# Kernel tuning notes

Measured on AMD Instinct MI355X. Metric: run time of the kernel, lower is better.

Reference implementation:

```python
import jax, jax.numpy as jnp
import numpy as np

EMBED_DIM = 1024
NUM_HEADS = 16
HEAD_DIM = EMBED_DIM // NUM_HEADS
B, S = 2, 2048


def setup_inputs() -> dict:
    key = jax.random.key(0)
    ks = jax.random.split(key, 9)
    s = 1.0 / np.sqrt(EMBED_DIM)
    return {
        "x": jax.random.normal(ks[0], (B, S, EMBED_DIM), dtype=jnp.float32),
        "Wq": jax.random.normal(ks[1], (EMBED_DIM, EMBED_DIM), dtype=jnp.float32) * s,
        "bq": jnp.zeros((EMBED_DIM,), dtype=jnp.float32),
        "Wk": jax.random.normal(ks[2], (EMBED_DIM, EMBED_DIM), dtype=jnp.float32) * s,
        "bk": jnp.zeros((EMBED_DIM,), dtype=jnp.float32),
        "Wv": jax.random.normal(ks[3], (EMBED_DIM, EMBED_DIM), dtype=jnp.float32) * s,
        "bv": jnp.zeros((EMBED_DIM,), dtype=jnp.float32),
        "Wo": jax.random.normal(ks[4], (EMBED_DIM, EMBED_DIM), dtype=jnp.float32) * s,
        "bo": jnp.zeros((EMBED_DIM,), dtype=jnp.float32),
    }


def reference(x, Wq, bq, Wk, bk, Wv, bv, Wo, bo):
    b, s, _ = x.shape
    # Projections; reshape to [B, H, S, Dh]
    def proj(W, bias):
        return (x @ W + bias).reshape(b, s, NUM_HEADS, HEAD_DIM).transpose(0, 2, 1, 3)
    q = proj(Wq, bq)
    k = proj(Wk, bk)
    v = proj(Wv, bv)
    scale = 1.0 / np.sqrt(HEAD_DIM).astype(np.float32)
    scores = jnp.einsum('bhqd,bhkd->bhqk', q, k) * scale  # [B,H,S,S]
    attn = jax.nn.softmax(scores, axis=-1)
    out = jnp.einsum('bhqk,bhkd->bhqd', attn, v)  # [B,H,S,Dh]
    out = out.transpose(0, 2, 1, 3).reshape(b, s, EMBED_DIM)
    return out @ Wo + bo
```

## Files before the change

kernel.cpp:

```cpp
#include <hip/hip_runtime.h>
#include <hip/hip_bf16.h>

typedef unsigned short ushort_t;
typedef __attribute__((ext_vector_type(8))) short short8;
typedef __attribute__((ext_vector_type(4))) float f32x4;
typedef __attribute__((ext_vector_type(16))) float f32x16;
typedef __attribute__((ext_vector_type(2))) unsigned int uint2v;

#define EMBED 1024
#define NHEAD 16
#define HDIM 64
#define BB 2
#define SSEQ 2048
#define MROWS (BB*SSEQ)
#define QKV_N (3*EMBED)
#define PER_BUF (MROWS*EMBED)

__device__ __forceinline__ ushort_t f2bf(float f) {
    union { float f; unsigned int u; } x; x.f = f;
    unsigned int r = x.u + 0x7fffu + ((x.u >> 16) & 1u);
    return (ushort_t)(r >> 16);
}
__device__ __forceinline__ unsigned cvt_pk_bf16(float lo, float hi) {
    unsigned r;
    asm("v_cvt_pk_bf16_f32 %0, %1, %2" : "=v"(r) : "v"(lo), "v"(hi));
    return r;
}

__device__ __forceinline__ void gload16(const void* g, void* l) {
    __builtin_amdgcn_global_load_lds(
        (const __attribute__((address_space(1))) unsigned int*)g,
        (__attribute__((address_space(3))) unsigned int*)l, 16, 0, 0);
}

__global__ void cast_bf16_kernel(const float* __restrict__ in, ushort_t* __restrict__ out, int n) {
    int i = (blockIdx.x * blockDim.x + threadIdx.x) * 4;
    if (i + 3 < n) {
        float4 v = *(const float4*)(in + i);
        out[i+0] = f2bf(v.x); out[i+1] = f2bf(v.y);
        out[i+2] = f2bf(v.z); out[i+3] = f2bf(v.w);
    }
}

__global__ void transpose_cast4_kernel(
    const float* __restrict__ W0, const float* __restrict__ W1,
    const float* __restrict__ W2, const float* __restrict__ W3,
    ushort_t* __restrict__ T0, ushort_t* __restrict__ T1,
    ushort_t* __restrict__ T2, ushort_t* __restrict__ T3)
{
    __shared__ float tile[32][33];
    int z = blockIdx.z;
    const float* W = (z == 0) ? W0 : (z == 1) ? W1 : (z == 2) ? W2 : W3;
    ushort_t* Wt   = (z == 0) ? T0 : (z == 1) ? T1 : (z == 2) ? T2 : T3;
    int tx = threadIdx.x, ty = threadIdx.y;
    int n0 = blockIdx.x * 32, k0 = blockIdx.y * 32;
    #pragma unroll
    for (int i = 0; i < 4; i++)
        tile[ty*4+i][tx] = W[(size_t)(k0 + ty*4 + i) * EMBED + n0 + tx];
    __syncthreads();
    #pragma unroll
    for (int i = 0; i < 4; i++)
        Wt[(size_t)(n0 + ty*4 + i) * EMBED + k0 + tx] = f2bf(tile[tx][ty*4+i]);
}

__global__ void transpose_v_kernel(const ushort_t* __restrict__ v, ushort_t* __restrict__ vt) {
    __shared__ ushort_t tile[64][66];
    int bh = blockIdx.y, s0 = blockIdx.x * 64;
    int t = threadIdx.x;
    int r = t >> 3, c8 = (t & 7) * 8;
    #pragma unroll
    for (int p = 0; p < 2; p++) {
        short8 vv = *(const short8*)&v[((size_t)bh*SSEQ + s0 + p*32 + r)*HDIM + c8];
        #pragma unroll
        for (int j = 0; j < 8; j++) tile[p*32 + r][c8 + j] = (ushort_t)vv[j];
    }
    __syncthreads();
    #pragma unroll
    for (int p = 0; p < 2; p++) {
        int d = p*32 + r;
        short8 ov;
        #pragma unroll
        for (int j = 0; j < 8; j++) ov[j] = (short)tile[c8 + j][d];
        *(short8*)&vt[((size_t)bh*HDIM + d)*SSEQ + s0 + c8] = ov;
    }
}

template<int OUT_MODE>
__global__ __launch_bounds__(256) void gemm_bt_kernel(
    const ushort_t* __restrict__ A,
    const ushort_t* __restrict__ Bt,
    const float* __restrict__ b0, const float* __restrict__ b1, const float* __restrict__ b2,
    void* __restrict__ Cout,
    int M, int N, int K)
{
    __shared__ __attribute__((aligned(16))) ushort_t Asm[128*64];
    __shared__ __attribute__((aligned(16))) ushort_t Bsm[128*64];
    int t = threadIdx.x;
    int w = t >> 6, l = t & 63;
    int wr = w >> 1, wc = w & 1;
    int lrow = l & 15, lhi = l >> 4;

    int gx = gridDim.x;
    int flat = blockIdx.y * gx + blockIdx.x;
    int q8 = (gx * gridDim.y) >> 3;
    int nf = (flat & 7) * q8 + (flat >> 3);
    int m0 = (nf / gx) * 128, n0 = (nf % gx) * 128;

    int srow8 = l >> 3;
    int colel = 8 * ((l & 7) ^ srow8);

    f32x4 acc[4][4];
    #pragma unroll
    for (int mi = 0; mi < 4; mi++)
        #pragma unroll
        for (int ni = 0; ni < 4; ni++)
            #pragma unroll
            for (int c = 0; c < 4; c++) acc[mi][ni][c] = 0.f;

    for (int k0 = 0; k0 < K; k0 += 64) {
        __syncthreads();
        #pragma unroll
        for (int p = 0; p < 4; p++) {
            int row = w*32 + p*8 + srow8;
            gload16(&A [(size_t)(m0 + row)*K + k0 + colel], &Asm[(w*32 + p*8)*64]);
            gload16(&Bt[(size_t)(n0 + row)*K + k0 + colel], &Bsm[(w*32 + p*8)*64]);
        }
        __syncthreads();
        #pragma unroll
        for (int kk = 0; kk < 2; kk++) {
            short8 af[4], bfr[4];
            #pragma unroll
            for (int mi = 0; mi < 4; mi++) {
                int r = wr*64 + mi*16 + lrow;
                af[mi] = *(short8*)&Asm[r*64 + ((kk*32 + lhi*8) ^ ((r & 7) << 3))];
            }
            #pragma unroll
            for (int ni = 0; ni < 4; ni++) {
                int r = wc*64 + ni*16 + lrow;
                bfr[ni] = *(short8*)&Bsm[r*64 + ((kk*32 + lhi*8) ^ ((r & 7) << 3))];
            }
            __builtin_amdgcn_s_setprio(1);
            #pragma unroll
            for (int mi = 0; mi < 4; mi++)
                #pragma unroll
                for (int ni = 0; ni < 4; ni++)
                    acc[mi][ni] = __builtin_amdgcn_mfma_f32_16x16x32_bf16(af[mi], bfr[ni], acc[mi][ni], 0, 0, 0);
            __builtin_amdgcn_s_setprio(0);
        }
    }

    #pragma unroll
    for (int mi = 0; mi < 4; mi++)
        #pragma unroll
        for (int ni = 0; ni < 4; ni++) {
            int col = n0 + wc*64 + ni*16 + lrow;
            #pragma unroll
            for (int c = 0; c < 4; c++) {
                int row = m0 + wr*64 + mi*16 + lhi*4 + c;
                if (OUT_MODE == 0) {
                    float v = acc[mi][ni][c] + b0[col];
                    ((float*)Cout)[(size_t)row * N + col] = v;
                } else {
                    int which = col >> 10, hc = col & 1023;
                    const float* bp = (which == 0) ? b0 : (which == 1) ? b1 : b2;
                    float v = acc[mi][ni][c] + bp[hc];
                    if (which == 0) v *= 0.18033688011112042f;
                    int h = hc >> 6, d = hc & 63;
                    int b = row >> 11, s = row & 2047;
                    ((ushort_t*)Cout)[(size_t)which*PER_BUF + ((size_t)((b*NHEAD + h)*SSEQ) + s)*HDIM + d] = f2bf(v);
                }
            }
        }
}

#define MFMA32(a,b,c) __builtin_amdgcn_mfma_f32_32x32x16_bf16(a, b, c, 0, 0, 0)

__global__ __launch_bounds__(256, 2) void flash_attn2_kernel(
    const ushort_t* __restrict__ q,
    const ushort_t* __restrict__ k,
    const ushort_t* __restrict__ vt,
    ushort_t* __restrict__ o)
{
    __shared__ __attribute__((aligned(16))) ushort_t Ks[2][2][64*64];
    __shared__ __attribute__((aligned(16))) ushort_t Vs[2][2][64*64];

    int t = threadIdx.x, w = t >> 6, l = t & 63;
    int l31 = l & 31, hi = l >> 5;

    int flat = blockIdx.x;
    int wg = (flat & 7) * 64 + (flat >> 3);
    int bh = wg >> 4;
    int q0 = (wg & 15) * 128;

    const ushort_t* qp = q  + (size_t)bh * SSEQ * HDIM;
    const ushort_t* kp = k  + (size_t)bh * SSEQ * HDIM;
    const ushort_t* vp = vt + (size_t)bh * HDIM * SSEQ;

    int lr = l >> 3, lc = l & 7;
    int colel = 8 * (lc ^ lr);

    short8 qf[4];
    int qrow = q0 + w*32 + l31;
    #pragma unroll
    for (int st = 0; st < 4; st++)
        qf[st] = *(const short8*)&qp[(size_t)qrow*HDIM + st*16 + hi*8];

    f32x16 o0 = {}, o1 = {};
    float m_run = -1e30f, l_run = 0.f;

    #define STAGE(buf, kv0) { \
        _Pragma("unroll") \
        for (int sub = 0; sub < 2; sub++) { \
            _Pragma("unroll") \
            for (int c = 0; c < 2; c++) { \
                int row = w*16 + c*8 + lr; \
                gload16(&kp[(size_t)(kv0 + sub*64 + row)*HDIM + colel], &Ks[buf][sub][(w*16 + c*8)*64]); \
                gload16(&vp[(size_t)row*SSEQ + (kv0) + sub*64 + colel], &Vs[buf][sub][(w*16 + c*8)*64]); \
            } } }

    STAGE(0, 0)
    asm volatile("s_waitcnt vmcnt(0)");
    __syncthreads();
    int cur = 0;

    for (int kv0 = 0; kv0 < SSEQ; kv0 += 128) {
        if (kv0 + 128 < SSEQ) { STAGE(cur ^ 1, kv0 + 128) }

        f32x16 s0 = {}, s1 = {}, s2 = {}, s3 = {};
        __builtin_amdgcn_s_setprio(1);
        #pragma unroll
        for (int st = 0; st < 4; st++) {
            int colb = st*16 + hi*8;
            int sw0 = colb ^ ((l31 & 7) << 3);
            short8 kf0 = *(const short8*)&Ks[cur][0][l31*64        + sw0];
            short8 kf1 = *(const short8*)&Ks[cur][0][(32 + l31)*64 + sw0];
            short8 kf2 = *(const short8*)&Ks[cur][1][l31*64        + sw0];
            short8 kf3 = *(const short8*)&Ks[cur][1][(32 + l31)*64 + sw0];
            s0 = MFMA32(kf0, qf[st], s0);
            s1 = MFMA32(kf1, qf[st], s1);
            s2 = MFMA32(kf2, qf[st], s2);
            s3 = MFMA32(kf3, qf[st], s3);
        }
        __builtin_amdgcn_s_setprio(0);

        float ma = fmaxf(s0[0], s0[1]);
        float mb = fmaxf(s0[2], s0[3]);
        float mc = fmaxf(s0[4], s0[5]);
        float md = fmaxf(s0[6], s0[7]);
        ma = fmaxf(fmaxf(ma, s0[8]),  s0[9]);
        mb = fmaxf(fmaxf(mb, s0[10]), s0[11]);
        mc = fmaxf(fmaxf(mc, s0[12]), s0[13]);
        md = fmaxf(fmaxf(md, s0[14]), s0[15]);
        ma = fmaxf(fmaxf(ma, s1[0]),  s1[1]);
        mb = fmaxf(fmaxf(mb, s1[2]),  s1[3]);
        mc = fmaxf(fmaxf(mc, s1[4]),  s1[5]);
        md = fmaxf(fmaxf(md, s1[6]),  s1[7]);
        ma = fmaxf(fmaxf(ma, s1[8]),  s1[9]);
        mb = fmaxf(fmaxf(mb, s1[10]), s1[11]);
        mc = fmaxf(fmaxf(mc, s1[12]), s1[13]);
        md = fmaxf(fmaxf(md, s1[14]), s1[15]);
        ma = fmaxf(fmaxf(ma, s2[0]),  s2[1]);
        mb = fmaxf(fmaxf(mb, s2[2]),  s2[3]);
        mc = fmaxf(fmaxf(mc, s2[4]),  s2[5]);
        md = fmaxf(fmaxf(md, s2[6]),  s2[7]);
        ma = fmaxf(fmaxf(ma, s2[8]),  s2[9]);
        mb = fmaxf(fmaxf(mb, s2[10]), s2[11]);
        mc = fmaxf(fmaxf(mc, s2[12]), s2[13]);
        md = fmaxf(fmaxf(md, s2[14]), s2[15]);
        ma = fmaxf(fmaxf(ma, s3[0]),  s3[1]);
        mb = fmaxf(fmaxf(mb, s3[2]),  s3[3]);
        mc = fmaxf(fmaxf(mc, s3[4]),  s3[5]);
        md = fmaxf(fmaxf(md, s3[6]),  s3[7]);
        ma = fmaxf(fmaxf(ma, s3[8]),  s3[9]);
        mb = fmaxf(fmaxf(mb, s3[10]), s3[11]);
        mc = fmaxf(fmaxf(mc, s3[12]), s3[13]);
        md = fmaxf(fmaxf(md, s3[14]), s3[15]);
        float mx = fmaxf(fmaxf(ma, mb), fmaxf(mc, md));
        mx = fmaxf(mx, __shfl_xor(mx, 32));

        if (__any(mx > m_run + 8.f)) {
            float mnew = fmaxf(m_run, mx);
            float alpha = __builtin_amdgcn_exp2f(m_run - mnew);
            #pragma unroll
            for (int r = 0; r < 16; r++) { o0[r] *= alpha; o1[r] *= alpha; }
            l_run *= alpha;
            m_run = mnew;
        }
        float r0 = 0.f, r1 = 0.f, r2 = 0.f, r3 = 0.f;
        #pragma unroll
        for (int r = 0; r < 16; r += 4) {
            s0[r]   = __builtin_amdgcn_exp2f(s0[r]   - m_run); r0 += s0[r];
            s0[r+1] = __builtin_amdgcn_exp2f(s0[r+1] - m_run); r1 += s0[r+1];
            s0[r+2] = __builtin_amdgcn_exp2f(s0[r+2] - m_run); r2 += s0[r+2];
            s0[r+3] = __builtin_amdgcn_exp2f(s0[r+3] - m_run); r3 += s0[r+3];
        }
        #pragma unroll
        for (int r = 0; r < 16; r += 4) {
            s1[r]   = __builtin_amdgcn_exp2f(s1[r]   - m_run); r0 += s1[r];
            s1[r+1] = __builtin_amdgcn_exp2f(s1[r+1] - m_run); r1 += s1[r+1];
            s1[r+2] = __builtin_amdgcn_exp2f(s1[r+2] - m_run); r2 += s1[r+2];
            s1[r+3] = __builtin_amdgcn_exp2f(s1[r+3] - m_run); r3 += s1[r+3];
        }
        #pragma unroll
        for (int r = 0; r < 16; r += 4) {
            s2[r]   = __builtin_amdgcn_exp2f(s2[r]   - m_run); r0 += s2[r];
            s2[r+1] = __builtin_amdgcn_exp2f(s2[r+1] - m_run); r1 += s2[r+1];
            s2[r+2] = __builtin_amdgcn_exp2f(s2[r+2] - m_run); r2 += s2[r+2];
            s2[r+3] = __builtin_amdgcn_exp2f(s2[r+3] - m_run); r3 += s2[r+3];
        }
        #pragma unroll
        for (int r = 0; r < 16; r += 4) {
            s3[r]   = __builtin_amdgcn_exp2f(s3[r]   - m_run); r0 += s3[r];
            s3[r+1] = __builtin_amdgcn_exp2f(s3[r+1] - m_run); r1 += s3[r+1];
            s3[r+2] = __builtin_amdgcn_exp2f(s3[r+2] - m_run); r2 += s3[r+2];
            s3[r+3] = __builtin_amdgcn_exp2f(s3[r+3] - m_run); r3 += s3[r+3];
        }
        float rs = (r0 + r1) + (r2 + r3);
        rs += __shfl_xor(rs, 32);
        l_run += rs;

        short8 pfr[8];
        #define PACK8(SV, KS0) { \
            unsigned a0 = cvt_pk_bf16(SV[0], SV[1]); \
            unsigned a1 = cvt_pk_bf16(SV[2], SV[3]); \
            unsigned b0 = cvt_pk_bf16(SV[4], SV[5]); \
            unsigned b1 = cvt_pk_bf16(SV[6], SV[7]); \
            uint2v rr0 = __builtin_amdgcn_permlane32_swap(a0, b0, false, false); \
            uint2v rr1 = __builtin_amdgcn_permlane32_swap(a1, b1, false, false); \
            union { unsigned u[4]; short8 v; } pfa; \
            pfa.u[0] = rr0.x; pfa.u[1] = rr1.x; pfa.u[2] = rr0.y; pfa.u[3] = rr1.y; \
            pfr[KS0] = pfa.v; \
            unsigned c0 = cvt_pk_bf16(SV[8], SV[9]); \
            unsigned c1 = cvt_pk_bf16(SV[10], SV[11]); \
            unsigned d0 = cvt_pk_bf16(SV[12], SV[13]); \
            unsigned d1 = cvt_pk_bf16(SV[14], SV[15]); \
            uint2v rr2 = __builtin_amdgcn_permlane32_swap(c0, d0, false, false); \
            uint2v rr3 = __builtin_amdgcn_permlane32_swap(c1, d1, false, false); \
            union { unsigned u[4]; short8 v; } pfb; \
            pfb.u[0] = rr2.x; pfb.u[1] = rr3.x; pfb.u[2] = rr2.y; pfb.u[3] = rr3.y; \
            pfr[(KS0)+1] = pfb.v; \
        }
        PACK8(s0, 0)
        PACK8(s1, 2)
        PACK8(s2, 4)
        PACK8(s3, 6)
        #undef PACK8

        __builtin_amdgcn_s_setprio(1);
        #pragma unroll
        for (int ks = 0; ks < 8; ks++) {
            int sub = ks >> 2;
            int colb = (ks & 3)*16 + hi*8;
            int sw = colb ^ ((l31 & 7) << 3);
            short8 vf0 = *(const short8*)&Vs[cur][sub][l31*64        + sw];
            short8 vf1 = *(const short8*)&Vs[cur][sub][(32 + l31)*64 + sw];
            o0 = MFMA32(vf0, pfr[ks], o0);
            o1 = MFMA32(vf1, pfr[ks], o1);
        }
        __builtin_amdgcn_s_setprio(0);

        asm volatile("s_waitcnt vmcnt(0)");
        __syncthreads();
        cur ^= 1;
    }

    float rl = 1.f / l_run;
    ushort_t* Ot = ((ushort_t*)Ks) + w*(32*64);
    #pragma unroll
    for (int dt = 0; dt < 2; dt++)
        #pragma unroll
        for (int rq = 0; rq < 4; rq++) {
            float v0 = (dt ? o1[rq*4+0] : o0[rq*4+0]) * rl;
            float v1 = (dt ? o1[rq*4+1] : o0[rq*4+1]) * rl;
            float v2 = (dt ? o1[rq*4+2] : o0[rq*4+2]) * rl;
            float v3 = (dt ? o1[rq*4+3] : o0[rq*4+3]) * rl;
            int d0 = dt*32 + rq*8 + hi*4;
            uint2v pw = { cvt_pk_bf16(v0, v1), cvt_pk_bf16(v2, v3) };
            *(uint2v*)&Ot[l31*64 + (d0 ^ ((l31 & 7) << 3))] = pw;
        }

    int b = bh >> 4, h = bh & 15;
    int q2 = l >> 1, dh = (l & 1) * 32;
    size_t obase = ((size_t)(b*SSEQ) + q0 + w*32 + q2)*EMBED + h*HDIM;
    #pragma unroll
    for (int j = 0; j < 4; j++) {
        int d = dh + j*8;
        short8 ov = *(short8*)&Ot[q2*64 + (d ^ ((q2 & 7) << 3))];
        *(short8*)&o[obase + d] = ov;
    }
}

extern "C" void kernel_launch(void* const* d_in, const int* in_sizes, int n_in,
                              void* d_out, int out_size, void* d_ws, size_t ws_size,
                              hipStream_t stream) {
    const float* x  = (const float*)d_in[0];
    const float* Wq = (const float*)d_in[1];
    const float* bq = (const float*)d_in[2];
    const float* Wk = (const float*)d_in[3];
    const float* bk = (const float*)d_in[4];
    const float* Wv = (const float*)d_in[5];
    const float* bv = (const float*)d_in[6];
    const float* Wo = (const float*)d_in[7];
    const float* bo = (const float*)d_in[8];

    char* ws = (char*)d_ws;
    ushort_t* xb  = (ushort_t*)(ws);
    ushort_t* WqT = (ushort_t*)(ws + (8u  << 20));
    ushort_t* WkT = (ushort_t*)(ws + (10u << 20));
    ushort_t* WvT = (ushort_t*)(ws + (12u << 20));
    ushort_t* WoT = (ushort_t*)(ws + (14u << 20));
    ushort_t* qb  = (ushort_t*)(ws + (16u << 20));
    ushort_t* kb  = (ushort_t*)(ws + (24u << 20));
    ushort_t* vb  = (ushort_t*)(ws + (32u << 20));
    ushort_t* vtb = (ushort_t*)(ws + (40u << 20));
    ushort_t* ab  = xb;

    int nx = MROWS * EMBED;
    cast_bf16_kernel<<<nx/(256*4), 256, 0, stream>>>(x, xb, nx);

    transpose_cast4_kernel<<<dim3(EMBED/32, EMBED/32, 4), dim3(32, 8), 0, stream>>>(
        Wq, Wk, Wv, Wo, WqT, WkT, WvT, WoT);

    gemm_bt_kernel<2><<<dim3(QKV_N/128, MROWS/128), 256, 0, stream>>>(
        xb, WqT, bq, bk, bv, qb, MROWS, QKV_N, EMBED);

    transpose_v_kernel<<<dim3(SSEQ/64, BB*NHEAD), 256, 0, stream>>>(vb, vtb);

    flash_attn2_kernel<<<512, 256, 0, stream>>>(qb, kb, vtb, ab);

    gemm_bt_kernel<0><<<dim3(EMBED/128, MROWS/128), 256, 0, stream>>>(
        ab, WoT, bo, bo, bo, d_out, MROWS, EMBED, EMBED);
}
```

Before: 122.4 us.

## Fuse V transpose into QKV GEMM epilogue and double attention block size

New measurement: 121.2 us (median of 2 runs). Within noise of the previous version (-1.0%).

```diff
diff --git a/kernel.cpp b/kernel.cpp
--- a/kernel.cpp
+++ b/kernel.cpp
@@ -2,6 +2,7 @@
 #include <hip/hip_bf16.h>
 
 typedef unsigned short ushort_t;
+typedef __attribute__((ext_vector_type(4))) short short4v;
 typedef __attribute__((ext_vector_type(8))) short short8;
 typedef __attribute__((ext_vector_type(4))) float f32x4;
 typedef __attribute__((ext_vector_type(16))) float f32x16;
@@ -63,34 +64,13 @@
         Wt[(size_t)(n0 + ty*4 + i) * EMBED + k0 + tx] = f2bf(tile[tx][ty*4+i]);
 }
 
-__global__ void transpose_v_kernel(const ushort_t* __restrict__ v, ushort_t* __restrict__ vt) {
-    __shared__ ushort_t tile[64][66];
-    int bh = blockIdx.y, s0 = blockIdx.x * 64;
-    int t = threadIdx.x;
-    int r = t >> 3, c8 = (t & 7) * 8;
-    #pragma unroll
-    for (int p = 0; p < 2; p++) {
-        short8 vv = *(const short8*)&v[((size_t)bh*SSEQ + s0 + p*32 + r)*HDIM + c8];
-        #pragma unroll
-        for (int j = 0; j < 8; j++) tile[p*32 + r][c8 + j] = (ushort_t)vv[j];
-    }
-    __syncthreads();
-    #pragma unroll
-    for (int p = 0; p < 2; p++) {
-        int d = p*32 + r;
-        short8 ov;
-        #pragma unroll
-        for (int j = 0; j < 8; j++) ov[j] = (short)tile[c8 + j][d];
-        *(short8*)&vt[((size_t)bh*HDIM + d)*SSEQ + s0 + c8] = ov;
-    }
-}
-
 template<int OUT_MODE>
 __global__ __launch_bounds__(256) void gemm_bt_kernel(
     const ushort_t* __restrict__ A,
     const ushort_t* __restrict__ Bt,
     const float* __restrict__ b0, const float* __restrict__ b1, const float* __restrict__ b2,
     void* __restrict__ Cout,
+    ushort_t* __restrict__ vt_out,
     int M, int N, int K)
 {
     __shared__ __attribute__((aligned(16))) ushort_t Asm[128*64];
@@ -154,20 +134,33 @@
         #pragma unroll
         for (int ni = 0; ni < 4; ni++) {
             int col = n0 + wc*64 + ni*16 + lrow;
-            #pragma unroll
-            for (int c = 0; c < 4; c++) {
-                int row = m0 + wr*64 + mi*16 + lhi*4 + c;
-                if (OUT_MODE == 0) {
-                    float v = acc[mi][ni][c] + b0[col];
-                    ((float*)Cout)[(size_t)row * N + col] = v;
-                } else {
-                    int which = col >> 10, hc = col & 1023;
-                    const float* bp = (which == 0) ? b0 : (which == 1) ? b1 : b2;
-                    float v = acc[mi][ni][c] + bp[hc];
-                    if (which == 0) v *= 0.18033688011112042f;
-                    int h = hc >> 6, d = hc & 63;
-                    int b = row >> 11, s = row & 2047;
-                    ((ushort_t*)Cout)[(size_t)which*PER_BUF + ((size_t)((b*NHEAD + h)*SSEQ) + s)*HDIM + d] = f2bf(v);
+            if (OUT_MODE == 2 && (col >> 10) == 2) {
+                int hc = col & 1023;
+                int h = hc >> 6, d = hc & 63;
+                int row0 = m0 + wr*64 + mi*16 + lhi*4;
+                int b = row0 >> 11, s0 = row0 & 2047;
+                int bh = b*NHEAD + h;
+                short4v pk;
+                #pragma unroll
+                for (int c = 0; c < 4; c++)
+                    pk[c] = (short)f2bf(acc[mi][ni][c] + b2[hc]);
+                *(short4v*)&vt_out[((size_t)bh*HDIM + d)*SSEQ + s0] = pk;
+            } else {
+                #pragma unroll
+                for (int c = 0; c < 4; c++) {
+                    int row = m0 + wr*64 + mi*16 + lhi*4 + c;
+                    if (OUT_MODE == 0) {
+                        float v = acc[mi][ni][c] + b0[col];
+                        ((float*)Cout)[(size_t)row * N + col] = v;
+                    } else {
+                        int which = col >> 10, hc = col & 1023;
+                        const float* bp = (which == 0) ? b0 : b1;
+                        float v = acc[mi][ni][c] + bp[hc];
+                        if (which == 0) v *= 0.18033688011112042f;
+                        int h = hc >> 6, d = hc & 63;
+                        int b = row >> 11, s = row & 2047;
+                        ((ushort_t*)Cout)[(size_t)which*PER_BUF + ((size_t)((b*NHEAD + h)*SSEQ) + s)*HDIM + d] = f2bf(v);
+                    }
                 }
             }
         }
@@ -175,7 +168,7 @@
 
 #define MFMA32(a,b,c) __builtin_amdgcn_mfma_f32_32x32x16_bf16(a, b, c, 0, 0, 0)
 
-__global__ __launch_bounds__(256, 2) void flash_attn2_kernel(
+__global__ __launch_bounds__(512, 1) void flash_attn2_kernel(
     const ushort_t* __restrict__ q,
     const ushort_t* __restrict__ k,
     const ushort_t* __restrict__ vt,
@@ -188,9 +181,9 @@
     int l31 = l & 31, hi = l >> 5;
 
     int flat = blockIdx.x;
-    int wg = (flat & 7) * 64 + (flat >> 3);
-    int bh = wg >> 4;
-    int q0 = (wg & 15) * 128;
+    int wg = (flat & 7) * 32 + (flat >> 3);
+    int bh = wg >> 3;
+    int q0 = (wg & 7) * 256;
 
     const ushort_t* qp = q  + (size_t)bh * SSEQ * HDIM;
     const ushort_t* kp = k  + (size_t)bh * SSEQ * HDIM;
@@ -211,12 +204,10 @@
     #define STAGE(buf, kv0) { \
         _Pragma("unroll") \
         for (int sub = 0; sub < 2; sub++) { \
-            _Pragma("unroll") \
-            for (int c = 0; c < 2; c++) { \
-                int row = w*16 + c*8 + lr; \
-                gload16(&kp[(size_t)(kv0 + sub*64 + row)*HDIM + colel], &Ks[buf][sub][(w*16 + c*8)*64]); \
-                gload16(&vp[(size_t)row*SSEQ + (kv0) + sub*64 + colel], &Vs[buf][sub][(w*16 + c*8)*64]); \
-            } } }
+            int row = w*8 + lr; \
+            gload16(&kp[(size_t)(kv0 + sub*64 + row)*HDIM + colel], &Ks[buf][sub][(w*8)*64]); \
+            gload16(&vp[(size_t)row*SSEQ + (kv0) + sub*64 + colel], &Vs[buf][sub][(w*8)*64]); \
+        } }
 
     STAGE(0, 0)
     asm volatile("s_waitcnt vmcnt(0)");
@@ -411,7 +402,6 @@
     ushort_t* WoT = (ushort_t*)(ws + (14u << 20));
     ushort_t* qb  = (ushort_t*)(ws + (16u << 20));
     ushort_t* kb  = (ushort_t*)(ws + (24u << 20));
-    ushort_t* vb  = (ushort_t*)(ws + (32u << 20));
     ushort_t* vtb = (ushort_t*)(ws + (40u << 20));
     ushort_t* ab  = xb;
 
@@ -422,12 +412,10 @@
         Wq, Wk, Wv, Wo, WqT, WkT, WvT, WoT);
 
     gemm_bt_kernel<2><<<dim3(QKV_N/128, MROWS/128), 256, 0, stream>>>(
-        xb, WqT, bq, bk, bv, qb, MROWS, QKV_N, EMBED);
-
-    transpose_v_kernel<<<dim3(SSEQ/64, BB*NHEAD), 256, 0, stream>>>(vb, vtb);
-
-    flash_attn2_kernel<<<512, 256, 0, stream>>>(qb, kb, vtb, ab);
+        xb, WqT, bq, bk, bv, qb, vtb, MROWS, QKV_N, EMBED);
+
+    flash_attn2_kernel<<<256, 512, 0, stream>>>(qb, kb, vtb, ab);
 
     gemm_bt_kernel<0><<<dim3(EMBED/128, MROWS/128), 256, 0, stream>>>(
-        ab, WoT, bo, bo, bo, d_out, MROWS, EMBED, EMBED);
-}
+        ab, WoT, bo, bo, bo, d_out, nullptr, MROWS, EMBED, EMBED);
+}
```
